# Performance work log

Measured on AMD Instinct MI355X. Metric: run time of the kernel, lower is better.

The kernel has to match this reference:

```python
import jax, jax.numpy as jnp
import numpy as np

NUM_WIRES = 4
NUM_LAYERS = 2
BATCH = 1_048_576


def _rz(theta):
    # diag(e^{-i t/2}, e^{+i t/2})
    e = jnp.exp(-0.5j * theta.astype(jnp.complex64))
    z = jnp.zeros((), jnp.complex64)
    return jnp.stack([jnp.stack([e, z]), jnp.stack([z, jnp.conj(e)])])


def _rx(theta):
    c = jnp.cos(0.5 * theta).astype(jnp.complex64)
    s = (-1j * jnp.sin(0.5 * theta)).astype(jnp.complex64)
    return jnp.stack([jnp.stack([c, s]), jnp.stack([s, c])])


def _apply_1q(state, U, w):
    # state: (B,2,2,2,2); apply 2x2 unitary U on wire w (axis w+1)
    s = jnp.moveaxis(state, w + 1, -1)
    s = jnp.einsum('...i,ji->...j', s, U)
    return jnp.moveaxis(s, -1, w + 1)


def _cnot(state, c, t):
    # flip target axis where control bit == 1
    s = jnp.moveaxis(state, (c + 1, t + 1), (-2, -1))
    s = jnp.stack([s[..., 0, :], s[..., 1, ::-1]], axis=-2)
    return jnp.moveaxis(s, (-2, -1), (c + 1, t + 1))


def _circuit(x, params):
    # RY(x_i)|0> per wire gives product state [cos(x_i/2), sin(x_i/2)]
    h = 0.5 * x
    a = jnp.stack([jnp.cos(h), jnp.sin(h)], axis=-1).astype(jnp.complex64)  # (B,4,2)
    state = jnp.einsum('bi,bj,bk,bl->bijkl', a[:, 0], a[:, 1], a[:, 2], a[:, 3])
    for layer in range(NUM_LAYERS):
        for w in range(NUM_WIRES):
            # RZ then RX on wire w, fused into one 2x2 unitary
            U = _rx(params[layer, w, 1]) @ _rz(params[layer, w, 0])
            state = _apply_1q(state, U, w)
        for w in range(NUM_WIRES - 1):
            state = _cnot(state, w, w + 1)
        state = _cnot(state, NUM_WIRES - 1, 0)
    probs = state.real ** 2 + state.imag ** 2  # (B,2,2,2,2)
    evs = []
    for w in range(NUM_WIRES):
        axes = tuple(ax for ax in range(1, NUM_WIRES + 1) if ax != w + 1)
        p = jnp.sum(probs, axis=axes)  # (B,2) marginal of wire w
        evs.append(p[:, 0] - p[:, 1])  # <Z_w>
    return jnp.stack(evs, axis=-1)  # (B,4)


def setup_inputs() -> dict:
    key = jax.random.key(0)
    k1, k2 = jax.random.split(key)
    x = jax.random.normal(k1, (BATCH, NUM_WIRES), dtype=jnp.float32)
    params = jax.random.normal(k2, (NUM_LAYERS, NUM_WIRES, 2), dtype=jnp.float32)
    return {"x": x, "params": params}


def reference(x, params):
    return _circuit(x, params)
```

## Files before the change

kernel.cpp:

```cpp
#include <hip/hip_runtime.h>

#define NUM_WIRES 4
#define NUM_LAYERS 2


__global__ void gate_prep(const float* __restrict__ params, float* __restrict__ g) {
    const int t = threadIdx.x;
    if (t < NUM_LAYERS * NUM_WIRES) {
        const float p0 = params[t * 2 + 0];
        const float p1 = params[t * 2 + 1];
        float cz, sz, cx, sx;
        __sincosf(0.5f * p0, &sz, &cz);
        __sincosf(0.5f * p1, &sx, &cx);
        float* G = g + t * 8;
        G[0] = cx * cz;   G[1] = -cx * sz;
        G[2] = sx * sz;   G[3] = -sx * cz;
        G[4] = -sx * sz;  G[5] = -sx * cz;
        G[6] = cx * cz;   G[7] = cx * sz;
    }
}

__device__ __forceinline__ void gate_factor(float c, float s, const float* __restrict__ G,
                                            float& v0r, float& v0i, float& v1r, float& v1i) {
    v0r = fmaf(G[0], c, G[2] * s);
    v0i = fmaf(G[1], c, G[3] * s);
    v1r = fmaf(G[4], c, G[6] * s);
    v1i = fmaf(G[5], c, G[7] * s);
}

__device__ __forceinline__ void cmul(float ar, float ai, float br, float bi,
                                     float& orr, float& oi) {
    orr = fmaf(ar, br, -ai * bi);
    oi  = fmaf(ar, bi,  ai * br);
}

template <int M>
__device__ __forceinline__ void apply_1q(float sr[16], float si[16], const float* __restrict__ G) {
    const float u00r = G[0], u00i = G[1], u01r = G[2], u01i = G[3];
    const float u10r = G[4], u10i = G[5], u11r = G[6], u11i = G[7];
#pragma unroll
    for (int i = 0; i < 16; ++i) {
        if (!(i & M)) {
            const int j = i | M;
            const float ar = sr[i], ai = si[i];
            const float br = sr[j], bi = si[j];
            sr[i] = fmaf(u00r, ar, fmaf(-u00i, ai, fmaf(u01r, br, -u01i * bi)));
            si[i] = fmaf(u00i, ar, fmaf(u00r, ai, fmaf(u01i, br, u01r * bi)));
            sr[j] = fmaf(u10r, ar, fmaf(-u10i, ai, fmaf(u11r, br, -u11i * bi)));
            si[j] = fmaf(u10i, ar, fmaf(u10r, ai, fmaf(u11i, br, u11r * bi)));
        }
    }
}

template <int CM, int TM>
__device__ __forceinline__ void cnot(float sr[16], float si[16]) {
#pragma unroll
    for (int i = 0; i < 16; ++i) {
        if ((i & CM) && !(i & TM)) {
            const int j = i | TM;
            float t;
            t = sr[i]; sr[i] = sr[j]; sr[j] = t;
            t = si[i]; si[i] = si[j]; si[j] = t;
        }
    }
}

__global__ __launch_bounds__(256) void qsim_kernel(const float* __restrict__ x,
                                                   const float* __restrict__ g,
                                                   float* __restrict__ out, int batch) {
    const int b = blockIdx.x * 256 + threadIdx.x;
    if (b >= batch) return;

    const float4 xv = reinterpret_cast<const float4*>(x)[b];

    float w0r[2], w0i[2], w1r[2], w1i[2], w2r[2], w2i[2], w3r[2], w3i[2];
    {
        float c, s;
        __sincosf(0.5f * xv.x, &s, &c);
        gate_factor(c, s, g + 0,  w0r[0], w0i[0], w0r[1], w0i[1]);
        __sincosf(0.5f * xv.y, &s, &c);
        gate_factor(c, s, g + 8,  w1r[0], w1i[0], w1r[1], w1i[1]);
        __sincosf(0.5f * xv.z, &s, &c);
        gate_factor(c, s, g + 16, w2r[0], w2i[0], w2r[1], w2i[1]);
        __sincosf(0.5f * xv.w, &s, &c);
        gate_factor(c, s, g + 24, w3r[0], w3i[0], w3r[1], w3i[1]);
    }

    float mr[4], mi[4], nr[4], ni[4];
#pragma unroll
    for (int p = 0; p < 2; ++p)
#pragma unroll
        for (int q = 0; q < 2; ++q) {
            cmul(w0r[p], w0i[p], w1r[q], w1i[q], mr[p * 2 + q], mi[p * 2 + q]);
            cmul(w2r[p], w2i[p], w3r[q], w3i[q], nr[p * 2 + q], ni[p * 2 + q]);
        }

    float sr[16], si[16];
#pragma unroll
    for (int i = 0; i < 16; ++i)
        cmul(mr[i >> 2], mi[i >> 2], nr[i & 3], ni[i & 3], sr[i], si[i]);

    cnot<8, 4>(sr, si);
    cnot<4, 2>(sr, si);
    cnot<2, 1>(sr, si);
    cnot<1, 8>(sr, si);

    apply_1q<8>(sr, si, g + 32);
    apply_1q<4>(sr, si, g + 40);
    apply_1q<2>(sr, si, g + 48);
    apply_1q<1>(sr, si, g + 56);
    cnot<8, 4>(sr, si);
    cnot<4, 2>(sr, si);
    cnot<2, 1>(sr, si);
    cnot<1, 8>(sr, si);

    float p[16];
#pragma unroll
    for (int i = 0; i < 16; ++i) p[i] = fmaf(sr[i], sr[i], si[i] * si[i]);

    float d0[8], s1[8];
#pragma unroll
    for (int k = 0; k < 8; ++k) { d0[k] = p[2 * k] - p[2 * k + 1]; s1[k] = p[2 * k] + p[2 * k + 1]; }
    const float e3 = ((d0[0] + d0[1]) + (d0[2] + d0[3])) + ((d0[4] + d0[5]) + (d0[6] + d0[7]));
    const float e2 = ((s1[0] - s1[1]) + (s1[2] - s1[3])) + ((s1[4] - s1[5]) + (s1[6] - s1[7]));
    float s2[4];
#pragma unroll
    for (int k = 0; k < 4; ++k) s2[k] = s1[2 * k] + s1[2 * k + 1];
    const float e1 = (s2[0] - s2[1]) + (s2[2] - s2[3]);
    const float e0 = (s2[0] + s2[1]) - (s2[2] + s2[3]);

    reinterpret_cast<float4*>(out)[b] = make_float4(e0, e1, e2, e3);
}

extern "C" void kernel_launch(void* const* d_in, const int* in_sizes, int n_in,
                              void* d_out, int out_size, void* d_ws, size_t ws_size,
                              hipStream_t stream) {
    const float* x = (const float*)d_in[0];
    const float* params = (const float*)d_in[1];
    float* out = (float*)d_out;
    float* g = (float*)d_ws;
    const int batch = in_sizes[0] / NUM_WIRES;

    gate_prep<<<1, 64, 0, stream>>>(params, g);
    const int blocks = (batch + 255) / 256;
    qsim_kernel<<<blocks, 256, 0, stream>>>(x, g, out, batch);
}
```

Before: 81.49 us.

## Factor second-layer gates into diagonal RZ phase and real-cos RX, use packed float2 math

Second-layer RZ rotations are folded into one precomputed diagonal phase vector of 16 complex entries, applied with a single complex multiply per amplitude. The RX gates then use only cos/sin, which cuts the FMA count per gate pair. All complex arithmetic moves to 2-wide float vectors so the compiler can emit packed FP32 instructions. This adds more gate_prep setup and relies on the compiler actually packing the vector ops.

```diff
diff --git a/kernel.cpp b/kernel.cpp
--- a/kernel.cpp
+++ b/kernel.cpp
@@ -3,10 +3,12 @@
 #define NUM_WIRES 4
 #define NUM_LAYERS 2
 
+typedef float v2 __attribute__((ext_vector_type(2)));
+
 
 __global__ void gate_prep(const float* __restrict__ params, float* __restrict__ g) {
     const int t = threadIdx.x;
-    if (t < NUM_LAYERS * NUM_WIRES) {
+    if (t < 4) {
         const float p0 = params[t * 2 + 0];
         const float p1 = params[t * 2 + 1];
         float cz, sz, cx, sx;
@@ -17,110 +19,126 @@
         G[2] = sx * sz;   G[3] = -sx * cz;
         G[4] = -sx * sz;  G[5] = -sx * cz;
         G[6] = cx * cz;   G[7] = cx * sz;
+    } else if (t < 8) {
+        const int w = t - 4;
+        const float p1 = params[(NUM_WIRES + w) * 2 + 1];
+        float cx, sx;
+        __sincosf(0.5f * p1, &sx, &cx);
+        g[32 + w * 2] = cx;
+        g[33 + w * 2] = sx;
+    } else if (t >= 16 && t < 32) {
+        const int i = t - 16;
+        float dr = 1.f, di = 0.f;
+        for (int w = 0; w < NUM_WIRES; ++w) {
+            const float p0 = params[(NUM_WIRES + w) * 2 + 0];
+            float c, s;
+            __sincosf(0.5f * p0, &s, &c);
+            const float sg = ((i >> (3 - w)) & 1) ? s : -s;
+            const float ndr = dr * c - di * sg;
+            const float ndi = dr * sg + di * c;
+            dr = ndr; di = ndi;
+        }
+        g[40 + i * 2] = dr;
+        g[41 + i * 2] = di;
     }
 }
 
-__device__ __forceinline__ void gate_factor(float c, float s, const float* __restrict__ G,
-                                            float& v0r, float& v0i, float& v1r, float& v1i) {
-    v0r = fmaf(G[0], c, G[2] * s);
-    v0i = fmaf(G[1], c, G[3] * s);
-    v1r = fmaf(G[4], c, G[6] * s);
-    v1i = fmaf(G[5], c, G[7] * s);
-}
+__device__ __forceinline__ v2 mk(float a, float b) { v2 r; r.x = a; r.y = b; return r; }
 
-__device__ __forceinline__ void cmul(float ar, float ai, float br, float bi,
-                                     float& orr, float& oi) {
-    orr = fmaf(ar, br, -ai * bi);
-    oi  = fmaf(ar, bi,  ai * br);
-}
-
-template <int M>
-__device__ __forceinline__ void apply_1q(float sr[16], float si[16], const float* __restrict__ G) {
-    const float u00r = G[0], u00i = G[1], u01r = G[2], u01i = G[3];
-    const float u10r = G[4], u10i = G[5], u11r = G[6], u11i = G[7];
-#pragma unroll
-    for (int i = 0; i < 16; ++i) {
-        if (!(i & M)) {
-            const int j = i | M;
-            const float ar = sr[i], ai = si[i];
-            const float br = sr[j], bi = si[j];
-            sr[i] = fmaf(u00r, ar, fmaf(-u00i, ai, fmaf(u01r, br, -u01i * bi)));
-            si[i] = fmaf(u00i, ar, fmaf(u00r, ai, fmaf(u01i, br, u01r * bi)));
-            sr[j] = fmaf(u10r, ar, fmaf(-u10i, ai, fmaf(u11r, br, -u11i * bi)));
-            si[j] = fmaf(u10i, ar, fmaf(u10r, ai, fmaf(u11i, br, u11r * bi)));
-        }
-    }
+__device__ __forceinline__ v2 cmul(v2 a, v2 b) {
+    const v2 t = mk(-a.y, a.y) * mk(b.y, b.x);
+    return __builtin_elementwise_fma(mk(a.x, a.x), b, t);
 }
 
 template <int CM, int TM>
-__device__ __forceinline__ void cnot(float sr[16], float si[16]) {
+__device__ __forceinline__ void cnot(v2 z[16]) {
 #pragma unroll
     for (int i = 0; i < 16; ++i) {
         if ((i & CM) && !(i & TM)) {
             const int j = i | TM;
-            float t;
-            t = sr[i]; sr[i] = sr[j]; sr[j] = t;
-            t = si[i]; si[i] = si[j]; si[j] = t;
+            const v2 t = z[i]; z[i] = z[j]; z[j] = t;
         }
     }
 }
 
 __global__ __launch_bounds__(256) void qsim_kernel(const float* __restrict__ x,
-                                                   const float* __restrict__ g,
+                                                   const float* __restrict__ gf,
                                                    float* __restrict__ out, int batch) {
     const int b = blockIdx.x * 256 + threadIdx.x;
     if (b >= batch) return;
+    const v2* __restrict__ g = (const v2*)gf;
 
     const float4 xv = reinterpret_cast<const float4*>(x)[b];
 
-    float w0r[2], w0i[2], w1r[2], w1i[2], w2r[2], w2i[2], w3r[2], w3i[2];
+    v2 f[4][2];
     {
+        const float xs0 = xv.x, xs1 = xv.y, xs2 = xv.z, xs3 = xv.w;
         float c, s;
-        __sincosf(0.5f * xv.x, &s, &c);
-        gate_factor(c, s, g + 0,  w0r[0], w0i[0], w0r[1], w0i[1]);
-        __sincosf(0.5f * xv.y, &s, &c);
-        gate_factor(c, s, g + 8,  w1r[0], w1i[0], w1r[1], w1i[1]);
-        __sincosf(0.5f * xv.z, &s, &c);
-        gate_factor(c, s, g + 16, w2r[0], w2i[0], w2r[1], w2i[1]);
-        __sincosf(0.5f * xv.w, &s, &c);
-        gate_factor(c, s, g + 24, w3r[0], w3i[0], w3r[1], w3i[1]);
+        __sincosf(0.5f * xs0, &s, &c);
+        f[0][0] = __builtin_elementwise_fma(mk(c, c), g[0], mk(s, s) * g[1]);
+        f[0][1] = __builtin_elementwise_fma(mk(c, c), g[2], mk(s, s) * g[3]);
+        __sincosf(0.5f * xs1, &s, &c);
+        f[1][0] = __builtin_elementwise_fma(mk(c, c), g[4], mk(s, s) * g[5]);
+        f[1][1] = __builtin_elementwise_fma(mk(c, c), g[6], mk(s, s) * g[7]);
+        __sincosf(0.5f * xs2, &s, &c);
+        f[2][0] = __builtin_elementwise_fma(mk(c, c), g[8], mk(s, s) * g[9]);
+        f[2][1] = __builtin_elementwise_fma(mk(c, c), g[10], mk(s, s) * g[11]);
+        __sincosf(0.5f * xs3, &s, &c);
+        f[3][0] = __builtin_elementwise_fma(mk(c, c), g[12], mk(s, s) * g[13]);
+        f[3][1] = __builtin_elementwise_fma(mk(c, c), g[14], mk(s, s) * g[15]);
     }
 
-    float mr[4], mi[4], nr[4], ni[4];
+    v2 m[4], n[4];
 #pragma unroll
     for (int p = 0; p < 2; ++p)
 #pragma unroll
         for (int q = 0; q < 2; ++q) {
-            cmul(w0r[p], w0i[p], w1r[q], w1i[q], mr[p * 2 + q], mi[p * 2 + q]);
-            cmul(w2r[p], w2i[p], w3r[q], w3i[q], nr[p * 2 + q], ni[p * 2 + q]);
+            m[p * 2 + q] = cmul(f[0][p], f[1][q]);
+            n[p * 2 + q] = cmul(f[2][p], f[3][q]);
         }
+    v2 z[16];
+#pragma unroll
+    for (int i = 0; i < 16; ++i) z[i] = cmul(m[i >> 2], n[i & 3]);
 
-    float sr[16], si[16];
+    cnot<8, 4>(z);
+    cnot<4, 2>(z);
+    cnot<2, 1>(z);
+    cnot<1, 8>(z);
+
 #pragma unroll
-    for (int i = 0; i < 16; ++i)
-        cmul(mr[i >> 2], mi[i >> 2], nr[i & 3], ni[i & 3], sr[i], si[i]);
+    for (int i = 0; i < 16; ++i) z[i] = cmul(g[20 + i], z[i]);
 
-    cnot<8, 4>(sr, si);
-    cnot<4, 2>(sr, si);
-    cnot<2, 1>(sr, si);
-    cnot<1, 8>(sr, si);
+#pragma unroll
+    for (int w = 0; w < 4; ++w) {
+        const v2 cs = g[16 + w];
+        const float c = cs.x, s = cs.y;
+        const int M = 8 >> w;
+#pragma unroll
+        for (int i = 0; i < 16; ++i) {
+            if (!(i & M)) {
+                const int j = i | M;
+                const v2 a = z[i], bb = z[j];
+                z[i] = __builtin_elementwise_fma(mk(c, c), a,  mk(s, -s) * mk(bb.y, bb.x));
+                z[j] = __builtin_elementwise_fma(mk(c, c), bb, mk(s, -s) * mk(a.y, a.x));
+            }
+        }
+    }
 
-    apply_1q<8>(sr, si, g + 32);
-    apply_1q<4>(sr, si, g + 40);
-    apply_1q<2>(sr, si, g + 48);
-    apply_1q<1>(sr, si, g + 56);
-    cnot<8, 4>(sr, si);
-    cnot<4, 2>(sr, si);
-    cnot<2, 1>(sr, si);
-    cnot<1, 8>(sr, si);
+    cnot<8, 4>(z);
+    cnot<4, 2>(z);
+    cnot<2, 1>(z);
+    cnot<1, 8>(z);
 
     float p[16];
 #pragma unroll
-    for (int i = 0; i < 16; ++i) p[i] = fmaf(sr[i], sr[i], si[i] * si[i]);
+    for (int i = 0; i < 16; ++i) p[i] = fmaf(z[i].x, z[i].x, z[i].y * z[i].y);
 
     float d0[8], s1[8];
 #pragma unroll
-    for (int k = 0; k < 8; ++k) { d0[k] = p[2 * k] - p[2 * k + 1]; s1[k] = p[2 * k] + p[2 * k + 1]; }
+    for (int k = 0; k < 8; ++k) {
+        d0[k] = p[2 * k] - p[2 * k + 1];
+        s1[k] = p[2 * k] + p[2 * k + 1];
+    }
     const float e3 = ((d0[0] + d0[1]) + (d0[2] + d0[3])) + ((d0[4] + d0[5]) + (d0[6] + d0[7]));
     const float e2 = ((s1[0] - s1[1]) + (s1[2] - s1[3])) + ((s1[4] - s1[5]) + (s1[6] - s1[7]));
     float s2[4];
```

Measured after the change: 80.82 us. About the same (-0.8%).
